# Kernel optimization log

Measured on AMD Instinct MI355X. Metric: run time of the kernel, lower is better.

The kernel has to match this reference:

```python
import jax, jax.numpy as jnp
import numpy as np
from jax import lax

B, CIN, COUT, H, W = 16, 128, 128, 128, 128
KH, KW = 3, 3
BLK_O, BLK_I = 32, 32          # block sizes over (out_ch, in_ch); kernel dims fully covered
PRUNING_RATE = 0.75


def _make_block_mask():
    # Reproduces blocksparse(): keep (1 - pruning_rate) of the channel blocks.
    nbo, nbi = COUT // BLK_O, CIN // BLK_I
    n_blocks = nbo * nbi
    n_keep = int(round(n_blocks * (1.0 - PRUNING_RATE)))
    rng = np.random.default_rng(42)
    keep = np.zeros(n_blocks, dtype=np.float32)
    keep[rng.permutation(n_blocks)[:n_keep]] = 1.0
    blk = keep.reshape(nbo, nbi)                     # [4, 4]
    m = np.kron(blk, np.ones((BLK_O, BLK_I), np.float32))   # [COUT, CIN]
    m = np.broadcast_to(m[:, :, None, None], (COUT, CIN, KH, KW))
    return jnp.asarray(np.ascontiguousarray(m))


def setup_inputs() -> dict:
    key = jax.random.key(0)
    k1, k2, k3 = jax.random.split(key, 3)
    x = jax.random.normal(k1, (B, CIN, H, W), dtype=jnp.float32)
    weight = jax.random.normal(k2, (COUT, CIN, KH, KW), dtype=jnp.float32) * 0.05
    bias = jax.random.normal(k3, (COUT,), dtype=jnp.float32) * 0.05
    mask = _make_block_mask()
    return {"x": x, "weight": weight, "bias": bias, "mask": mask}


def reference(x, weight, bias, mask):
    # weight = weight * mask, then standard dense conv2d (stride 1, pad 1, dil 1, groups 1)
    w = weight * mask
    y = lax.conv_general_dilated(
        x, w,
        window_strides=(1, 1),
        padding=((1, 1), (1, 1)),
        dimension_numbers=("NCHW", "OIHW", "NCHW"),
    )
    return y + bias[None, :, None, None]
```

## Files before the change

### kernel.cpp

```cpp
#include <hip/hip_runtime.h>

#define NBATCH 16
#define CIN_ 128
#define COUT_ 128
#define H_ 128
#define W_ 128
#define TH 4
#define NR (TH + 2)
#define PSTRIDE 32

typedef short bf16x8 __attribute__((ext_vector_type(8)));
typedef float f32x4 __attribute__((ext_vector_type(4)));
typedef unsigned short u16x8 __attribute__((ext_vector_type(8)));

__device__ __forceinline__ unsigned short f32_to_bf16(float f) {
  unsigned int u = __float_as_uint(f);
  u += 0x7fffu + ((u >> 16) & 1u);
  return (unsigned short)(u >> 16);
}

__device__ __forceinline__ int mask_bits(const float* __restrict__ mask, int ob, int lane) {
  float mv = (lane < 4) ? mask[((size_t)(ob * 32) * CIN_ + lane * 32) * 9] : 0.0f;
  unsigned long long bal = __ballot(mv != 0.0f);
  return (int)(bal & 15ull);
}

__global__ __launch_bounds__(256) void pack_w_k(const float* __restrict__ weight,
                                                const float* __restrict__ mask,
                                                unsigned short* __restrict__ wpack) {
  const int khkw = blockIdx.x;
  const int slot = blockIdx.y;
  const int ob   = blockIdx.z;
  const int mb = mask_bits(mask, ob, threadIdx.x & 63);
  if (slot >= __popc(mb)) return;
  int m = mb;
  for (int t = 0; t < slot; ++t) m &= m - 1;
  const int ib = __ffs(m) - 1;
  const int kh = khkw / 3, kw = khkw % 3;
  for (int e = threadIdx.x; e < 1024; e += 256) {
    const int co = e >> 5, ci = e & 31;
    const int cog = ob * 32 + co, cig = ib * 32 + ci;
    const size_t widx = ((size_t)(cog * CIN_ + cig) * 3 + kh) * 3 + kw;
    const float v = weight[widx] * mask[widx];
    wpack[(size_t)((ob * 4 + slot) * 9 + khkw) * 1024 + e] = f32_to_bf16(v);
  }
}

__global__ __launch_bounds__(256, 3) void conv_fused_k(const float* __restrict__ x,
                                                       const unsigned short* __restrict__ wpack,
                                                       const float* __restrict__ mask,
                                                       const float* __restrict__ bias,
                                                       float* __restrict__ out) {
  __shared__ __align__(16) unsigned short xs[NR * 130 * PSTRIDE];

  const int tid  = threadIdx.x;
  const int wave = tid >> 6;
  const int lane = tid & 63;
  const int wl   = lane & 15;
  const int kg   = lane >> 4;

  const int h0 = blockIdx.x * TH;
  const int b  = blockIdx.y;
  const int ob = blockIdx.z;
  const int w0 = wave * 32;

  const int mb  = mask_bits(mask, ob, lane);
  const int cnt = __popc(mb);

  f32x4 acc[TH][2][2] = {};

  const int g   = tid & 7;
  const int q   = tid >> 3;
  const int oct = g & 3;

  int mrem = mb;
  for (int s = 0; s < cnt; ++s) {
    const int ib = __ffs(mrem) - 1;
    mrem &= mrem - 1;

    if (s) __syncthreads();

    {
      const float* xbase =
          x + ((size_t)b * CIN_ + ib * 32 + oct * 8) * H_ * W_ + q * 4;
#pragma unroll
      for (int it = 0; it < 3; ++it) {
        const int r = it * 2 + (g >> 2);
        const int row = h0 - 1 + r;
        const bool rv = (row >= 0) && (row < H_);
        const float* src = xbase + (size_t)(rv ? row : 0) * W_;
        f32x4 v0 = *(const f32x4*)(src);
        f32x4 v1 = *(const f32x4*)(src + 1 * (size_t)H_ * W_);
        f32x4 v2 = *(const f32x4*)(src + 2 * (size_t)H_ * W_);
        f32x4 v3 = *(const f32x4*)(src + 3 * (size_t)H_ * W_);
        f32x4 v4 = *(const f32x4*)(src + 4 * (size_t)H_ * W_);
        f32x4 v5 = *(const f32x4*)(src + 5 * (size_t)H_ * W_);
        f32x4 v6 = *(const f32x4*)(src + 6 * (size_t)H_ * W_);
        f32x4 v7 = *(const f32x4*)(src + 7 * (size_t)H_ * W_);
#pragma unroll
        for (int j = 0; j < 4; ++j) {
          u16x8 o;
          if (rv) {
            o[0] = f32_to_bf16(v0[j]); o[1] = f32_to_bf16(v1[j]);
            o[2] = f32_to_bf16(v2[j]); o[3] = f32_to_bf16(v3[j]);
            o[4] = f32_to_bf16(v4[j]); o[5] = f32_to_bf16(v5[j]);
            o[6] = f32_to_bf16(v6[j]); o[7] = f32_to_bf16(v7[j]);
          } else {
            o = u16x8{0, 0, 0, 0, 0, 0, 0, 0};
          }
          *(u16x8*)(xs + (r * 130 + q * 4 + 1 + j) * PSTRIDE + oct * 8) = o;
        }
      }
      for (int e = tid; e < NR * 2 * 32; e += 256) {
        const int r = e >> 6, edge = (e >> 5) & 1, cc = e & 31;
        xs[(r * 130 + (edge ? 129 : 0)) * PSTRIDE + cc] = 0;
      }
    }

    const unsigned short* wk =
        wpack + (size_t)((ob * 4 + s) * 9) * 1024 + wl * 32 + kg * 8;
    bf16x8 a[3][3][2];
#pragma unroll
    for (int kh = 0; kh < 3; ++kh)
#pragma unroll
      for (int kw = 0; kw < 3; ++kw) {
        a[kh][kw][0] = *(const bf16x8*)(wk + (kh * 3 + kw) * 1024);
        a[kh][kw][1] = *(const bf16x8*)(wk + (kh * 3 + kw) * 1024 + 16 * 32);
      }

    __syncthreads();

#pragma unroll
    for (int ridx = 0; ridx < NR; ++ridx) {
      bf16x8 bf[2][3];
#pragma unroll
      for (int ni = 0; ni < 2; ++ni)
#pragma unroll
        for (int kw = 0; kw < 3; ++kw)
          bf[ni][kw] = *(const bf16x8*)(xs + (ridx * 130 + w0 + ni * 16 + wl + kw) * PSTRIDE + kg * 8);

#pragma unroll
      for (int kh = 0; kh < 3; ++kh) {
        const int hi = ridx - kh;
        if (hi < 0 || hi >= TH) continue;
#pragma unroll
        for (int kw = 0; kw < 3; ++kw) {
          acc[hi][0][0] = __builtin_amdgcn_mfma_f32_16x16x32_bf16(a[kh][kw][0], bf[0][kw], acc[hi][0][0], 0, 0, 0);
          acc[hi][0][1] = __builtin_amdgcn_mfma_f32_16x16x32_bf16(a[kh][kw][0], bf[1][kw], acc[hi][0][1], 0, 0, 0);
          acc[hi][1][0] = __builtin_amdgcn_mfma_f32_16x16x32_bf16(a[kh][kw][1], bf[0][kw], acc[hi][1][0], 0, 0, 0);
          acc[hi][1][1] = __builtin_amdgcn_mfma_f32_16x16x32_bf16(a[kh][kw][1], bf[1][kw], acc[hi][1][1], 0, 0, 0);
        }
      }
    }
  }

#pragma unroll
  for (int mi = 0; mi < 2; ++mi)
#pragma unroll
    for (int j = 0; j < 4; ++j) {
      const int co = mi * 16 + kg * 4 + j;
      const float bv = bias[ob * 32 + co];
#pragma unroll
      for (int hh = 0; hh < TH; ++hh) {
        float* yrow = out + ((size_t)(b * COUT_ + ob * 32 + co) * H_ + h0 + hh) * W_;
        __builtin_nontemporal_store(acc[hh][mi][0][j] + bv, yrow + w0 + wl);
        __builtin_nontemporal_store(acc[hh][mi][1][j] + bv, yrow + w0 + wl + 16);
      }
    }
}

extern "C" void kernel_launch(void* const* d_in, const int* in_sizes, int n_in,
                              void* d_out, int out_size, void* d_ws, size_t ws_size,
                              hipStream_t stream) {
  const float* x      = (const float*)d_in[0];
  const float* weight = (const float*)d_in[1];
  const float* bias   = (const float*)d_in[2];
  const float* mask   = (const float*)d_in[3];
  float* out = (float*)d_out;

  unsigned short* wpack = (unsigned short*)d_ws;

  pack_w_k<<<dim3(9, 4, 4), 256, 0, stream>>>(weight, mask, wpack);
  conv_fused_k<<<dim3(H_ / TH, NBATCH, 4), 256, 0, stream>>>(x, wpack, mask, bias, out);
}
```

Before: 87.83 us.

## Pad LDS pixel pitch and restructure input staging loads

Changes the shared-memory pixel pitch from 32 to 34 bf16 values, aiming to cut bank conflicts on the transposed writes. Input staging is remapped so each group of 32 threads reads a contiguous image row, and all global loads are issued into registers before the weight loads; the values are converted and packed into 32-bit LDS stores afterwards. Launch bounds drop from 3 to 2 blocks per SM, and output stores go from nontemporal to normal stores. The odd pitch leaves the 16-byte B-operand LDS reads misaligned, which may force split reads. The larger register arrays also reduce occupancy.

```diff
diff --git a/kernel.cpp b/kernel.cpp
--- a/kernel.cpp
+++ b/kernel.cpp
@@ -7,11 +7,10 @@
 #define W_ 128
 #define TH 4
 #define NR (TH + 2)
-#define PSTRIDE 32
+#define CPITCH 34
 
 typedef short bf16x8 __attribute__((ext_vector_type(8)));
 typedef float f32x4 __attribute__((ext_vector_type(4)));
-typedef unsigned short u16x8 __attribute__((ext_vector_type(8)));
 
 __device__ __forceinline__ unsigned short f32_to_bf16(float f) {
   unsigned int u = __float_as_uint(f);
@@ -46,12 +45,12 @@
   }
 }
 
-__global__ __launch_bounds__(256, 3) void conv_fused_k(const float* __restrict__ x,
+__global__ __launch_bounds__(256, 2) void conv_fused_k(const float* __restrict__ x,
                                                        const unsigned short* __restrict__ wpack,
                                                        const float* __restrict__ mask,
                                                        const float* __restrict__ bias,
                                                        float* __restrict__ out) {
-  __shared__ __align__(16) unsigned short xs[NR * 130 * PSTRIDE];
+  __shared__ unsigned short xs[NR * 130 * CPITCH];
 
   const int tid  = threadIdx.x;
   const int wave = tid >> 6;
@@ -69,9 +68,8 @@
 
   f32x4 acc[TH][2][2] = {};
 
-  const int g   = tid & 7;
-  const int q   = tid >> 3;
-  const int oct = g & 3;
+  const int q = tid & 31;
+  const int g = tid >> 5;
 
   int mrem = mb;
   for (int s = 0; s < cnt; ++s) {
@@ -80,41 +78,18 @@
 
     if (s) __syncthreads();
 
-    {
-      const float* xbase =
-          x + ((size_t)b * CIN_ + ib * 32 + oct * 8) * H_ * W_ + q * 4;
+    const float* xbase = x + ((size_t)b * CIN_ + ib * 32) * H_ * W_ + q * 4;
+    f32x4 Ra[12], Rb[12];
 #pragma unroll
-      for (int it = 0; it < 3; ++it) {
-        const int r = it * 2 + (g >> 2);
-        const int row = h0 - 1 + r;
-        const bool rv = (row >= 0) && (row < H_);
-        const float* src = xbase + (size_t)(rv ? row : 0) * W_;
-        f32x4 v0 = *(const f32x4*)(src);
-        f32x4 v1 = *(const f32x4*)(src + 1 * (size_t)H_ * W_);
-        f32x4 v2 = *(const f32x4*)(src + 2 * (size_t)H_ * W_);
-        f32x4 v3 = *(const f32x4*)(src + 3 * (size_t)H_ * W_);
-        f32x4 v4 = *(const f32x4*)(src + 4 * (size_t)H_ * W_);
-        f32x4 v5 = *(const f32x4*)(src + 5 * (size_t)H_ * W_);
-        f32x4 v6 = *(const f32x4*)(src + 6 * (size_t)H_ * W_);
-        f32x4 v7 = *(const f32x4*)(src + 7 * (size_t)H_ * W_);
-#pragma unroll
-        for (int j = 0; j < 4; ++j) {
-          u16x8 o;
-          if (rv) {
-            o[0] = f32_to_bf16(v0[j]); o[1] = f32_to_bf16(v1[j]);
-            o[2] = f32_to_bf16(v2[j]); o[3] = f32_to_bf16(v3[j]);
-            o[4] = f32_to_bf16(v4[j]); o[5] = f32_to_bf16(v5[j]);
-            o[6] = f32_to_bf16(v6[j]); o[7] = f32_to_bf16(v7[j]);
-          } else {
-            o = u16x8{0, 0, 0, 0, 0, 0, 0, 0};
-          }
-          *(u16x8*)(xs + (r * 130 + q * 4 + 1 + j) * PSTRIDE + oct * 8) = o;
-        }
-      }
-      for (int e = tid; e < NR * 2 * 32; e += 256) {
-        const int r = e >> 6, edge = (e >> 5) & 1, cc = e & 31;
-        xs[(r * 130 + (edge ? 129 : 0)) * PSTRIDE + cc] = 0;
-      }
+    for (int it = 0; it < 12; ++it) {
+      const int combo = it * 8 + g;
+      const int r  = combo >> 4;
+      const int cp = combo & 15;
+      const int row = h0 - 1 + r;
+      const bool rv = (row >= 0) && (row < H_);
+      const float* src = xbase + ((size_t)(cp * 2) * H_ + (rv ? row : 0)) * W_;
+      Ra[it] = *(const f32x4*)src;
+      Rb[it] = *(const f32x4*)(src + (size_t)H_ * W_);
     }
 
     const unsigned short* wk =
@@ -128,6 +103,26 @@
         a[kh][kw][1] = *(const bf16x8*)(wk + (kh * 3 + kw) * 1024 + 16 * 32);
       }
 
+#pragma unroll
+    for (int it = 0; it < 12; ++it) {
+      const int combo = it * 8 + g;
+      const int r  = combo >> 4;
+      const int cp = combo & 15;
+      const int row = h0 - 1 + r;
+      const bool rv = (row >= 0) && (row < H_);
+      unsigned int* xd = (unsigned int*)(xs + (r * 130 + q * 4 + 1) * CPITCH + cp * 2);
+#pragma unroll
+      for (int j = 0; j < 4; ++j) {
+        unsigned int lo = rv ? (unsigned int)f32_to_bf16(Ra[it][j]) : 0u;
+        unsigned int hi = rv ? (unsigned int)f32_to_bf16(Rb[it][j]) : 0u;
+        xd[j * (CPITCH / 2)] = lo | (hi << 16);
+      }
+    }
+    for (int e = tid; e < NR * 2 * 32; e += 256) {
+      const int r = e >> 6, edge = (e >> 5) & 1, cc = e & 31;
+      xs[(r * 130 + (edge ? 129 : 0)) * CPITCH + cc] = 0;
+    }
+
     __syncthreads();
 
 #pragma unroll
@@ -137,7 +132,7 @@
       for (int ni = 0; ni < 2; ++ni)
 #pragma unroll
         for (int kw = 0; kw < 3; ++kw)
-          bf[ni][kw] = *(const bf16x8*)(xs + (ridx * 130 + w0 + ni * 16 + wl + kw) * PSTRIDE + kg * 8);
+          bf[ni][kw] = *(const bf16x8*)(xs + (ridx * 130 + w0 + ni * 16 + wl + kw) * CPITCH + kg * 8);
 
 #pragma unroll
       for (int kh = 0; kh < 3; ++kh) {
@@ -163,8 +158,8 @@
 #pragma unroll
       for (int hh = 0; hh < TH; ++hh) {
         float* yrow = out + ((size_t)(b * COUT_ + ob * 32 + co) * H_ + h0 + hh) * W_;
-        __builtin_nontemporal_store(acc[hh][mi][0][j] + bv, yrow + w0 + wl);
-        __builtin_nontemporal_store(acc[hh][mi][1][j] + bv, yrow + w0 + wl + 16);
+        yrow[w0 + wl]      = acc[hh][mi][0][j] + bv;
+        yrow[w0 + wl + 16] = acc[hh][mi][1][j] + bv;
       }
     }
 }
```

After: 96.06 us. +9.4%, slower.
